# Kernel tuning notes

Measured on AMD Instinct MI355X. Metric: run time of the kernel, lower is better.

The kernel has to match this reference:

```python
import jax, jax.numpy as jnp
import numpy as np
from jax.scipy.special import logsumexp

B, T, D, L = 64, 512, 1024, 16


def setup_inputs() -> dict:
    key = jax.random.key(0)
    ks = jax.random.split(key, 6)
    x = jax.random.normal(ks[0], (B, T, D), dtype=jnp.float32)
    mask = jnp.ones((B, T), dtype=bool)
    labels = jax.random.randint(ks[1], (B, T), 0, L)
    W = jax.random.normal(ks[2], (D, L), dtype=jnp.float32) * (1.0 / np.sqrt(D))
    b = jnp.zeros((L,), dtype=jnp.float32)
    transitions = jax.random.normal(ks[3], (L, L), dtype=jnp.float32) * 0.1
    start_trans = jax.random.normal(ks[4], (L,), dtype=jnp.float32) * 0.1
    end_trans = jax.random.normal(ks[5], (L,), dtype=jnp.float32) * 0.1
    return {"x": x, "mask": mask, "labels": labels, "W": W, "b": b,
            "transitions": transitions, "start_trans": start_trans, "end_trans": end_trans}


def _crf_loss(x, mask, labels, W, b, transitions, start_trans, end_trans):
    logits = jnp.einsum("btd,dl->btl", x, W) + b  # (B,T,L)
    maskf = mask.astype(logits.dtype)

    # ---- log partition via forward algorithm (scan over time) ----
    logits_t = jnp.swapaxes(logits, 0, 1)  # (T,B,L)
    mask_t = jnp.swapaxes(mask, 0, 1)      # (T,B)
    alpha0 = start_trans + logits_t[0]     # (B,L)

    def step(alpha, inp):
        emit, m = inp  # emit: (B,L), m: (B,)
        # transitions[i,j]: from tag i to tag j
        inner = alpha[:, :, None] + transitions[None, :, :] + emit[:, None, :]
        new = logsumexp(inner, axis=1)
        alpha = jnp.where(m[:, None], new, alpha)
        return alpha, None

    alpha, _ = jax.lax.scan(step, alpha0, (logits_t[1:], mask_t[1:]))
    log_z = logsumexp(alpha + end_trans, axis=-1)  # (B,)

    # ---- joint score of gold path ----
    emit = jnp.take_along_axis(logits, labels[..., None], axis=2)[..., 0]  # (B,T)
    emit_score = jnp.sum(emit * maskf, axis=1)
    trans = transitions[labels[:, :-1], labels[:, 1:]]  # (B,T-1)
    trans_score = jnp.sum(trans * maskf[:, 1:], axis=1)
    last_idx = jnp.sum(mask.astype(jnp.int32), axis=1) - 1  # (B,)
    last_tag = jnp.take_along_axis(labels, last_idx[:, None], axis=1)[:, 0]
    score = start_trans[labels[:, 0]] + emit_score + trans_score + end_trans[last_tag]

    log_likelihood = jnp.sum(score - log_z)
    return -log_likelihood  # loss


def reference(x, mask, labels, W, b, transitions, start_trans, end_trans):
    return _crf_loss(x, mask, labels, W, b, transitions, start_trans, end_trans)
```

## Files before the change

### kernel.cpp

```cpp
#include <hip/hip_runtime.h>

#define B_ 64
#define T_ 512
#define D_ 1024
#define L_ 16

__global__ __launch_bounds__(256) void crf_gemm(const float* __restrict__ x,
                                                const float* __restrict__ W,
                                                const float* __restrict__ bias,
                                                float* __restrict__ logits,
                                                float* __restrict__ outz) {
    if (blockIdx.x == 0 && threadIdx.x == 0) outz[0] = 0.f;
    const int l  = threadIdx.x & 63;
    const int kq = threadIdx.x >> 6;
    const int dq = l & 15;
    const int lq = l >> 4;
    const int dbase = kq * 256 + dq * 4;
    const int r0 = blockIdx.x * 16;

    __shared__ float part[4][16][16];

    float4 wreg[4][4];
#pragma unroll
    for (int c = 0; c < 4; ++c)
#pragma unroll
        for (int dd = 0; dd < 4; ++dd)
            wreg[c][dd] = *reinterpret_cast<const float4*>(
                &W[(size_t)(dbase + c * 64 + dd) * L_ + lq * 4]);

    float4 xn[4];
#pragma unroll
    for (int c = 0; c < 4; ++c)
        xn[c] = *reinterpret_cast<const float4*>(&x[(size_t)r0 * D_ + dbase + c * 64]);

    for (int r = 0; r < 16; ++r) {
        float4 xv[4];
#pragma unroll
        for (int c = 0; c < 4; ++c) xv[c] = xn[c];
        if (r < 15) {
#pragma unroll
            for (int c = 0; c < 4; ++c)
                xn[c] = *reinterpret_cast<const float4*>(
                    &x[(size_t)(r0 + r + 1) * D_ + dbase + c * 64]);
        }
        float a0 = 0.f, a1 = 0.f, a2 = 0.f, a3 = 0.f;
#pragma unroll
        for (int c = 0; c < 4; ++c) {
            float xs[4] = {xv[c].x, xv[c].y, xv[c].z, xv[c].w};
#pragma unroll
            for (int dd = 0; dd < 4; ++dd) {
                a0 = fmaf(xs[dd], wreg[c][dd].x, a0);
                a1 = fmaf(xs[dd], wreg[c][dd].y, a1);
                a2 = fmaf(xs[dd], wreg[c][dd].z, a2);
                a3 = fmaf(xs[dd], wreg[c][dd].w, a3);
            }
        }
        float v0, v1;
        {
            const int h = dq & 1;
            float k0 = h ? a1 : a0, s0 = h ? a0 : a1;
            float k1 = h ? a3 : a2, s1 = h ? a2 : a3;
            v0 = k0 + __shfl_xor(s0, 1);
            v1 = k1 + __shfl_xor(s1, 1);
        }
        {
            const int h = (dq >> 1) & 1;
            float k = h ? v1 : v0, s = h ? v0 : v1;
            v0 = k + __shfl_xor(s, 2);
        }
        v0 += __shfl_xor(v0, 4);
        v0 += __shfl_xor(v0, 8);
        if (dq < 4) part[kq][r][lq * 4 + dq] = v0;
    }
    __syncthreads();
    const int row = threadIdx.x >> 4;
    const int lab = threadIdx.x & 15;
    float s = part[0][row][lab] + part[1][row][lab] + part[2][row][lab] +
              part[3][row][lab] + bias[lab];
    logits[(size_t)(r0 + row) * L_ + lab] = s;
}

__global__ __launch_bounds__(1024) void crf_rest(const float* __restrict__ logits,
                                                 const int* __restrict__ labels,
                                                 const float* __restrict__ trans,
                                                 const float* __restrict__ startt,
                                                 const float* __restrict__ endt,
                                                 float* __restrict__ out) {
    __shared__ float P[16][256];
    __shared__ float Ss[16];
    __shared__ float scoreP[16];
    const int b = blockIdx.x;
    const int tid = threadIdx.x;
    const int w = tid >> 6;
    const int l = tid & 63;
    const int i = l & 15;
    const int jq = l >> 4;
    const float* lg = logits + (size_t)b * (T_ * L_);

    float4 etp[4][4];
#pragma unroll
    for (int g = 0; g < 4; ++g)
#pragma unroll
        for (int t = 0; t < 4; ++t) {
            int k = ((jq ^ g) << 2) + t;
            float4 tv = *reinterpret_cast<const float4*>(&trans[k * L_ + (jq << 2)]);
            etp[g][t] = make_float4(__expf(tv.x), __expf(tv.y), __expf(tv.z), __expf(tv.w));
        }

    float p0 = (i == (jq << 2) + 0) ? 1.f : 0.f;
    float p1 = (i == (jq << 2) + 1) ? 1.f : 0.f;
    float p2 = (i == (jq << 2) + 2) ? 1.f : 0.f;
    float p3 = (i == (jq << 2) + 3) ? 1.f : 0.f;
    float S = 0.f;

    const int t0 = w * 32;
    float4 emn = *reinterpret_cast<const float4*>(&lg[(size_t)t0 * L_ + (jq << 2)]);
#pragma unroll 4
    for (int s = 0; s < 32; ++s) {
        float4 em = emn;
        if (s < 31)
            emn = *reinterpret_cast<const float4*>(&lg[(size_t)(t0 + s + 1) * L_ + (jq << 2)]);
        if (t0 + s >= 1) {
            float mx = fmaxf(fmaxf(em.x, em.y), fmaxf(em.z, em.w));
            mx = fmaxf(mx, __shfl_xor(mx, 16));
            mx = fmaxf(mx, __shfl_xor(mx, 32));
            S += mx;
            float qx = __expf(em.x - mx), qy = __expf(em.y - mx);
            float qz = __expf(em.z - mx), qw = __expf(em.w - mx);
            float r[4][4];
            r[0][0] = p0; r[0][1] = p1; r[0][2] = p2; r[0][3] = p3;
#pragma unroll
            for (int g = 1; g < 4; ++g) {
                r[g][0] = __shfl_xor(p0, g << 4);
                r[g][1] = __shfl_xor(p1, g << 4);
                r[g][2] = __shfl_xor(p2, g << 4);
                r[g][3] = __shfl_xor(p3, g << 4);
            }
            float ax = 0.f, ay = 0.f, az = 0.f, aw = 0.f;
#pragma unroll
            for (int g = 0; g < 4; ++g)
#pragma unroll
                for (int t = 0; t < 4; ++t) {
                    ax = fmaf(r[g][t], etp[g][t].x, ax);
                    ay = fmaf(r[g][t], etp[g][t].y, ay);
                    az = fmaf(r[g][t], etp[g][t].z, az);
                    aw = fmaf(r[g][t], etp[g][t].w, aw);
                }
            ax *= qx; ay *= qy; az *= qz; aw *= qw;
            if ((s & 3) == 3) {
                float m = fmaxf(fmaxf(ax, ay), fmaxf(az, aw));
#pragma unroll
                for (int ww = 1; ww < 64; ww <<= 1) m = fmaxf(m, __shfl_xor(m, ww));
                unsigned eb = (__float_as_uint(m) >> 23) & 0xFFu;
                float scl = __uint_as_float((254u - eb) << 23);
                ax *= scl; ay *= scl; az *= scl; aw *= scl;
                S += ((int)eb - 127) * 0.69314718056f;
            }
            p0 = ax; p1 = ay; p2 = az; p3 = aw;
        }
    }
    *reinterpret_cast<float4*>(&P[w][i * 16 + (jq << 2)]) = make_float4(p0, p1, p2, p3);
    if (l == 0) Ss[w] = S;

    float sc = 0.f;
    if (tid < T_) {
        int lt = labels[b * T_ + tid];
        sc = lg[tid * L_ + lt];
        if (tid >= 1) sc += trans[labels[b * T_ + tid - 1] * L_ + lt];
    }
#pragma unroll
    for (int ww = 1; ww < 64; ww <<= 1) sc += __shfl_xor(sc, ww);
    if (l == 0) scoreP[w] = sc;
    __syncthreads();

    if (w == 0) {
        const int j = l & 15;
        const int kq = l >> 4;
        float a0 = startt[j] + lg[j];
        float m0 = a0;
#pragma unroll
        for (int ww = 1; ww < 16; ww <<= 1) m0 = fmaxf(m0, __shfl_xor(m0, ww));
        float v = __expf(a0 - m0);
        float S2 = m0;
        for (int c = 0; c < 16; ++c) {
            float cur[4];
#pragma unroll
            for (int t = 0; t < 4; ++t) cur[t] = P[c][(kq * 4 + t) * 16 + j];
            float pt = 0.f;
#pragma unroll
            for (int t = 0; t < 4; ++t)
                pt = fmaf(__shfl(v, (l & 48) + kq * 4 + t), cur[t], pt);
            pt += __shfl_xor(pt, 16);
            pt += __shfl_xor(pt, 32);
            S2 += Ss[c];
            if ((c & 3) == 3) {
                float m = pt;
#pragma unroll
                for (int ww = 1; ww < 16; ww <<= 1) m = fmaxf(m, __shfl_xor(m, ww));
                unsigned eb = (__float_as_uint(m) >> 23) & 0xFFu;
                pt *= __uint_as_float((254u - eb) << 23);
                S2 += ((int)eb - 127) * 0.69314718056f;
            }
            v = pt;
        }
        float term = v * __expf(endt[j]);
#pragma unroll
        for (int ww = 1; ww < 16; ww <<= 1) term += __shfl_xor(term, ww);
        float logz = S2 + __logf(term);
        if (l == 0) {
            float score = startt[labels[b * T_]] + endt[labels[b * T_ + T_ - 1]];
#pragma unroll
            for (int q = 0; q < 16; ++q) score += scoreP[q];
            atomicAdd(out, logz - score);
        }
    }
}

extern "C" void kernel_launch(void* const* d_in, const int* in_sizes, int n_in,
                              void* d_out, int out_size, void* d_ws, size_t ws_size,
                              hipStream_t stream) {
    const float* x      = (const float*)d_in[0];
    const int*   labels = (const int*)d_in[2];
    const float* W      = (const float*)d_in[3];
    const float* bias   = (const float*)d_in[4];
    const float* trans  = (const float*)d_in[5];
    const float* startt = (const float*)d_in[6];
    const float* endt   = (const float*)d_in[7];

    float* logits = (float*)d_ws;
    float* out    = (float*)d_out;

    crf_gemm<<<2048, 256, 0, stream>>>(x, W, bias, logits, out);
    crf_rest<<<64, 1024, 0, stream>>>(logits, labels, trans, startt, endt, out);
}
```

Before: 240.0 us.

## Split GEMM along D into eight slices with a separate partial-sum reduce kernel

```diff
diff --git a/kernel.cpp b/kernel.cpp
--- a/kernel.cpp
+++ b/kernel.cpp
@@ -5,79 +5,88 @@
 #define D_ 1024
 #define L_ 16
 
-__global__ __launch_bounds__(256) void crf_gemm(const float* __restrict__ x,
-                                                const float* __restrict__ W,
-                                                const float* __restrict__ bias,
-                                                float* __restrict__ logits,
-                                                float* __restrict__ outz) {
+__global__ __launch_bounds__(256, 6) void crf_gemm(const float* __restrict__ x,
+                                                   const float* __restrict__ W,
+                                                   float* __restrict__ partial,
+                                                   float* __restrict__ outz) {
     if (blockIdx.x == 0 && threadIdx.x == 0) outz[0] = 0.f;
     const int l  = threadIdx.x & 63;
-    const int kq = threadIdx.x >> 6;
-    const int dq = l & 15;
-    const int lq = l >> 4;
-    const int dbase = kq * 256 + dq * 4;
-    const int r0 = blockIdx.x * 16;
-
-    __shared__ float part[4][16][16];
-
-    float4 wreg[4][4];
-#pragma unroll
-    for (int c = 0; c < 4; ++c)
-#pragma unroll
-        for (int dd = 0; dd < 4; ++dd)
-            wreg[c][dd] = *reinterpret_cast<const float4*>(
-                &W[(size_t)(dbase + c * 64 + dd) * L_ + lq * 4]);
-
-    float4 xn[4];
-#pragma unroll
-    for (int c = 0; c < 4; ++c)
-        xn[c] = *reinterpret_cast<const float4*>(&x[(size_t)r0 * D_ + dbase + c * 64]);
-
-    for (int r = 0; r < 16; ++r) {
-        float4 xv[4];
-#pragma unroll
-        for (int c = 0; c < 4; ++c) xv[c] = xn[c];
-        if (r < 15) {
-#pragma unroll
-            for (int c = 0; c < 4; ++c)
-                xn[c] = *reinterpret_cast<const float4*>(
-                    &x[(size_t)(r0 + r + 1) * D_ + dbase + c * 64]);
-        }
-        float a0 = 0.f, a1 = 0.f, a2 = 0.f, a3 = 0.f;
-#pragma unroll
-        for (int c = 0; c < 4; ++c) {
-            float xs[4] = {xv[c].x, xv[c].y, xv[c].z, xv[c].w};
-#pragma unroll
-            for (int dd = 0; dd < 4; ++dd) {
-                a0 = fmaf(xs[dd], wreg[c][dd].x, a0);
-                a1 = fmaf(xs[dd], wreg[c][dd].y, a1);
-                a2 = fmaf(xs[dd], wreg[c][dd].z, a2);
-                a3 = fmaf(xs[dd], wreg[c][dd].w, a3);
-            }
-        }
-        float v0, v1;
-        {
-            const int h = dq & 1;
-            float k0 = h ? a1 : a0, s0 = h ? a0 : a1;
-            float k1 = h ? a3 : a2, s1 = h ? a2 : a3;
-            v0 = k0 + __shfl_xor(s0, 1);
-            v1 = k1 + __shfl_xor(s1, 1);
-        }
-        {
-            const int h = (dq >> 1) & 1;
-            float k = h ? v1 : v0, s = h ? v0 : v1;
-            v0 = k + __shfl_xor(s, 2);
-        }
-        v0 += __shfl_xor(v0, 4);
-        v0 += __shfl_xor(v0, 8);
-        if (dq < 4) part[kq][r][lq * 4 + dq] = v0;
-    }
-    __syncthreads();
-    const int row = threadIdx.x >> 4;
-    const int lab = threadIdx.x & 15;
-    float s = part[0][row][lab] + part[1][row][lab] + part[2][row][lab] +
-              part[3][row][lab] + bias[lab];
-    logits[(size_t)(r0 + row) * L_ + lab] = s;
+    const int gw = blockIdx.x * 4 + (threadIdx.x >> 6);
+    const int s  = gw & 7;
+    const int rb = gw >> 3;
+    const int d0 = s * 128 + l;
+
+    float4 w0[4], w1[4];
+#pragma unroll
+    for (int q = 0; q < 4; ++q) {
+        w0[q] = *reinterpret_cast<const float4*>(&W[(size_t)d0 * L_ + q * 4]);
+        w1[q] = *reinterpret_cast<const float4*>(&W[(size_t)(d0 + 64) * L_ + q * 4]);
+    }
+
+    const float* xr = x + (size_t)rb * 32 * D_;
+    float xa[2][4], xb[2][4];
+#pragma unroll
+    for (int rr = 0; rr < 4; ++rr) {
+        xa[0][rr] = xr[(size_t)rr * D_ + d0];
+        xb[0][rr] = xr[(size_t)rr * D_ + d0 + 64];
+    }
+
+    for (int g = 0; g < 8; ++g) {
+        const int cur = g & 1;
+        if (g < 7) {
+#pragma unroll
+            for (int rr = 0; rr < 4; ++rr) {
+                xa[cur ^ 1][rr] = xr[(size_t)((g + 1) * 4 + rr) * D_ + d0];
+                xb[cur ^ 1][rr] = xr[(size_t)((g + 1) * 4 + rr) * D_ + d0 + 64];
+            }
+        }
+#pragma unroll
+        for (int rr = 0; rr < 4; ++rr) {
+            const int row = rb * 32 + g * 4 + rr;
+            const float xv0 = xa[cur][rr], xv1 = xb[cur][rr];
+            float red[16];
+#pragma unroll
+            for (int q = 0; q < 4; ++q) {
+                red[q * 4 + 0] = fmaf(xv1, w1[q].x, xv0 * w0[q].x);
+                red[q * 4 + 1] = fmaf(xv1, w1[q].y, xv0 * w0[q].y);
+                red[q * 4 + 2] = fmaf(xv1, w1[q].z, xv0 * w0[q].z);
+                red[q * 4 + 3] = fmaf(xv1, w1[q].w, xv0 * w0[q].w);
+            }
+#pragma unroll
+            for (int bnum = 0; bnum < 4; ++bnum) {
+                const int m = 1 << bnum;
+                const int h = (l >> bnum) & 1;
+                const int n = 16 >> (bnum + 1);
+#pragma unroll
+                for (int t2 = 0; t2 < 8; ++t2) {
+                    if (t2 < n) {
+                        float keep = h ? red[2 * t2 + 1] : red[2 * t2];
+                        float send = h ? red[2 * t2] : red[2 * t2 + 1];
+                        red[t2] = keep + __shfl_xor(send, m);
+                    }
+                }
+            }
+            float v = red[0];
+            v += __shfl_xor(v, 16);
+            v += __shfl_xor(v, 32);
+            if (l < 16)
+                partial[((size_t)s * 32768 + row) * L_ + l] = v;
+        }
+    }
+}
+
+__global__ __launch_bounds__(64) void crf_reduce(const float* __restrict__ partial,
+                                                 const float* __restrict__ bias,
+                                                 float* __restrict__ logits) {
+    const int t = blockIdx.x * 64 + threadIdx.x;
+    const float4* p4 = reinterpret_cast<const float4*>(partial);
+    float4 o = reinterpret_cast<const float4*>(bias)[t & 3];
+#pragma unroll
+    for (int s = 0; s < 8; ++s) {
+        float4 a = p4[(size_t)s * 131072 + t];
+        o.x += a.x; o.y += a.y; o.z += a.z; o.w += a.w;
+    }
+    reinterpret_cast<float4*>(logits)[t] = o;
 }
 
 __global__ __launch_bounds__(1024) void crf_rest(const float* __restrict__ logits,
@@ -227,9 +236,12 @@
     const float* startt = (const float*)d_in[6];
     const float* endt   = (const float*)d_in[7];
 
-    float* logits = (float*)d_ws;
-    float* out    = (float*)d_out;
-
-    crf_gemm<<<2048, 256, 0, stream>>>(x, W, bias, logits, out);
+    float* ws      = (float*)d_ws;
+    float* partial = ws;
+    float* logits  = ws + 4194304;
+    float* out     = (float*)d_out;
+
+    crf_gemm<<<2048, 256, 0, stream>>>(x, W, partial, out);
+    crf_reduce<<<2048, 64, 0, stream>>>(partial, bias, logits);
     crf_rest<<<64, 1024, 0, stream>>>(logits, labels, trans, startt, endt, out);
 }
```

Result: slower. 265.8 us (+10.8%).

## Compute emission GEMM with bf16 MFMA and a prepacked W fragment buffer

Applied to the files above, without the earlier changes.

```diff
diff --git a/kernel.cpp b/kernel.cpp
--- a/kernel.cpp
+++ b/kernel.cpp
@@ -5,79 +5,75 @@
 #define D_ 1024
 #define L_ 16
 
+typedef __attribute__((ext_vector_type(8))) short short8;
+typedef __attribute__((ext_vector_type(4))) float f32x4;
+
+__device__ __forceinline__ unsigned bfpack(float lo, float hi) {
+    unsigned a = __float_as_uint(lo), b = __float_as_uint(hi);
+    a = (a + 0x7FFFu + ((a >> 16) & 1u)) >> 16;
+    b = (b + 0x7FFFu + ((b >> 16) & 1u)) & 0xFFFF0000u;
+    return a | b;
+}
+
+__global__ __launch_bounds__(256) void crf_wprep(const float* __restrict__ W,
+                                                 float* __restrict__ wfrag,
+                                                 float* __restrict__ outz) {
+    const int f = blockIdx.x * 256 + threadIdx.x;
+    if (f == 0) outz[0] = 0.f;
+    const int l = f & 63, n = l & 15, quad = l >> 4;
+    const int k0 = (f >> 6) * 32 + quad * 8;
+    unsigned u[4];
+#pragma unroll
+    for (int d = 0; d < 4; ++d)
+        u[d] = bfpack(W[(size_t)(k0 + 2 * d) * L_ + n],
+                      W[(size_t)(k0 + 2 * d + 1) * L_ + n]);
+    reinterpret_cast<uint4*>(wfrag)[f] = make_uint4(u[0], u[1], u[2], u[3]);
+}
+
 __global__ __launch_bounds__(256) void crf_gemm(const float* __restrict__ x,
-                                                const float* __restrict__ W,
+                                                const float* __restrict__ wfrag,
                                                 const float* __restrict__ bias,
-                                                float* __restrict__ logits,
-                                                float* __restrict__ outz) {
-    if (blockIdx.x == 0 && threadIdx.x == 0) outz[0] = 0.f;
-    const int l  = threadIdx.x & 63;
-    const int kq = threadIdx.x >> 6;
-    const int dq = l & 15;
-    const int lq = l >> 4;
-    const int dbase = kq * 256 + dq * 4;
-    const int r0 = blockIdx.x * 16;
-
-    __shared__ float part[4][16][16];
-
-    float4 wreg[4][4];
-#pragma unroll
-    for (int c = 0; c < 4; ++c)
-#pragma unroll
-        for (int dd = 0; dd < 4; ++dd)
-            wreg[c][dd] = *reinterpret_cast<const float4*>(
-                &W[(size_t)(dbase + c * 64 + dd) * L_ + lq * 4]);
-
-    float4 xn[4];
-#pragma unroll
-    for (int c = 0; c < 4; ++c)
-        xn[c] = *reinterpret_cast<const float4*>(&x[(size_t)r0 * D_ + dbase + c * 64]);
-
-    for (int r = 0; r < 16; ++r) {
-        float4 xv[4];
-#pragma unroll
-        for (int c = 0; c < 4; ++c) xv[c] = xn[c];
-        if (r < 15) {
-#pragma unroll
-            for (int c = 0; c < 4; ++c)
-                xn[c] = *reinterpret_cast<const float4*>(
-                    &x[(size_t)(r0 + r + 1) * D_ + dbase + c * 64]);
-        }
-        float a0 = 0.f, a1 = 0.f, a2 = 0.f, a3 = 0.f;
-#pragma unroll
-        for (int c = 0; c < 4; ++c) {
-            float xs[4] = {xv[c].x, xv[c].y, xv[c].z, xv[c].w};
-#pragma unroll
-            for (int dd = 0; dd < 4; ++dd) {
-                a0 = fmaf(xs[dd], wreg[c][dd].x, a0);
-                a1 = fmaf(xs[dd], wreg[c][dd].y, a1);
-                a2 = fmaf(xs[dd], wreg[c][dd].z, a2);
-                a3 = fmaf(xs[dd], wreg[c][dd].w, a3);
-            }
-        }
-        float v0, v1;
-        {
-            const int h = dq & 1;
-            float k0 = h ? a1 : a0, s0 = h ? a0 : a1;
-            float k1 = h ? a3 : a2, s1 = h ? a2 : a3;
-            v0 = k0 + __shfl_xor(s0, 1);
-            v1 = k1 + __shfl_xor(s1, 1);
-        }
-        {
-            const int h = (dq >> 1) & 1;
-            float k = h ? v1 : v0, s = h ? v0 : v1;
-            v0 = k + __shfl_xor(s, 2);
-        }
-        v0 += __shfl_xor(v0, 4);
-        v0 += __shfl_xor(v0, 8);
-        if (dq < 4) part[kq][r][lq * 4 + dq] = v0;
-    }
-    __syncthreads();
-    const int row = threadIdx.x >> 4;
-    const int lab = threadIdx.x & 15;
-    float s = part[0][row][lab] + part[1][row][lab] + part[2][row][lab] +
-              part[3][row][lab] + bias[lab];
-    logits[(size_t)(r0 + row) * L_ + lab] = s;
+                                                float* __restrict__ logits) {
+    const int l = threadIdx.x & 63;
+    const int wv = threadIdx.x >> 6;
+    const int quad = l >> 4;
+    const int n = l & 15;
+    const int r0 = (blockIdx.x * 4 + wv) * 16;
+
+    const float* xrow = x + (size_t)(r0 + n) * D_ + quad * 8;
+    const float4* wfp = reinterpret_cast<const float4*>(wfrag) + l;
+
+    float4 xa[4], xb[4], wf[4];
+#pragma unroll
+    for (int p = 0; p < 4; ++p) {
+        xa[p] = *reinterpret_cast<const float4*>(xrow + p * 32);
+        xb[p] = *reinterpret_cast<const float4*>(xrow + p * 32 + 4);
+        wf[p] = wfp[p * 64];
+    }
+
+    f32x4 acc = {0.f, 0.f, 0.f, 0.f};
+#pragma unroll
+    for (int kc = 0; kc < 32; ++kc) {
+        const int sl = kc & 3;
+        union { unsigned u[4]; short8 s; } a;
+        a.u[0] = bfpack(xa[sl].x, xa[sl].y);
+        a.u[1] = bfpack(xa[sl].z, xa[sl].w);
+        a.u[2] = bfpack(xb[sl].x, xb[sl].y);
+        a.u[3] = bfpack(xb[sl].z, xb[sl].w);
+        union { float4 f; short8 s; } b;
+        b.f = wf[sl];
+        if (kc < 28) {
+            xa[sl] = *reinterpret_cast<const float4*>(xrow + (kc + 4) * 32);
+            xb[sl] = *reinterpret_cast<const float4*>(xrow + (kc + 4) * 32 + 4);
+            wf[sl] = wfp[(kc + 4) * 64];
+        }
+        acc = __builtin_amdgcn_mfma_f32_16x16x32_bf16(a.s, b.s, acc, 0, 0, 0);
+    }
+
+    const float bb = bias[n];
+#pragma unroll
+    for (int r = 0; r < 4; ++r)
+        logits[(size_t)(r0 + quad * 4 + r) * L_ + n] = acc[r] + bb;
 }
 
 __global__ __launch_bounds__(1024) void crf_rest(const float* __restrict__ logits,
@@ -227,9 +223,12 @@
     const float* startt = (const float*)d_in[6];
     const float* endt   = (const float*)d_in[7];
 
-    float* logits = (float*)d_ws;
+    float* ws     = (float*)d_ws;
+    float* wfrag  = ws;
+    float* logits = ws + 8192;
     float* out    = (float*)d_out;
 
-    crf_gemm<<<2048, 256, 0, stream>>>(x, W, bias, logits, out);
+    crf_wprep<<<8, 256, 0, stream>>>(W, wfrag, out);
+    crf_gemm<<<512, 256, 0, stream>>>(x, wfrag, bias, logits);
     crf_rest<<<64, 1024, 0, stream>>>(logits, labels, trans, startt, endt, out);
 }
```

New measurement: 238.6 us. No clear change (-0.6%).
